# Kernel optimization log

Hardware: AMD Instinct MI355X
Metric: run time of the kernel (lower is better)

The kernel has to match this reference:

```python
import jax, jax.numpy as jnp
import numpy as np

D = 1024      # n_embd
NH = 16       # attention heads
E = 8         # n_experts
K = 2         # k_best
FF = 4 * D    # expert MLP hidden
EPS = 1e-6    # rms_norm_epsilon
TEMP = 1.0    # target_temperature


def setup_inputs() -> dict:
    key = jax.random.key(0)
    ks = jax.random.split(key, 12)
    B, S = 2, 1024
    s = 0.02
    return {
        "x": jax.random.normal(ks[0], (B, S, D), jnp.float32),
        "attn_norm_w": jnp.ones((D,), jnp.float32),
        "wq": jax.random.normal(ks[1], (D, D), jnp.float32) * s,
        "wk": jax.random.normal(ks[2], (D, D), jnp.float32) * s,
        "wv": jax.random.normal(ks[3], (D, D), jnp.float32) * s,
        "wo": jax.random.normal(ks[4], (D, D), jnp.float32) * s,
        "mlp_norm_w": jnp.ones((D,), jnp.float32),
        "router_w": jax.random.normal(ks[5], (D, E), jnp.float32) * s,
        "w1": jax.random.normal(ks[6], (E, D, FF), jnp.float32) * s,
        "b1": jnp.zeros((E, FF), jnp.float32),
        "w2": jax.random.normal(ks[7], (E, FF, D), jnp.float32) * s,
        "b2": jnp.zeros((E, D), jnp.float32),
    }


def _rmsnorm(x, w):
    var = jnp.mean(jnp.square(x), axis=-1, keepdims=True)
    return x * jax.lax.rsqrt(var + EPS) * w


def _attention(x, wq, wk, wv, wo):
    B, S, _ = x.shape
    dh = D // NH
    q = (x @ wq).reshape(B, S, NH, dh)
    k = (x @ wk).reshape(B, S, NH, dh)
    v = (x @ wv).reshape(B, S, NH, dh)
    scores = jnp.einsum("bqhd,bkhd->bhqk", q, k) / jnp.sqrt(jnp.float32(dh))
    causal = jnp.tril(jnp.ones((S, S), bool))  # [S,S]
    scores = jnp.where(causal[None, None], scores, jnp.finfo(scores.dtype).min)
    attn = jax.nn.softmax(scores, axis=-1)
    out = jnp.einsum("bhqk,bkhd->bqhd", attn, v).reshape(B, S, D)
    return out @ wo


def reference(x, attn_norm_w, wq, wk, wv, wo, mlp_norm_w, router_w, w1, b1, w2, b2):
    B, S, _ = x.shape
    # attention sub-block
    x = x + _attention(_rmsnorm(x, attn_norm_w), wq, wk, wv, wo)
    residual = x
    h = _rmsnorm(x, mlp_norm_w)  # [B,S,D]

    # router: temperature softmax + top-k
    logits = h @ router_w / TEMP                      # [B,S,E]
    probs = jax.nn.softmax(logits, axis=-1)
    top_k_scores, top_k_indices = jax.lax.top_k(probs, K)  # [B,S,K]
    onehot = jax.nn.one_hot(top_k_indices, E, dtype=h.dtype)  # [B,S,K,E]
    gates = jnp.einsum("bsk,bske->bse", top_k_scores, onehot)  # [B,S,E]

    # load-balancing loss (Switch-style) + expert counts
    counts = jnp.sum(onehot, axis=(0, 1, 2))          # [E]
    frac = counts / (B * S * K)
    mean_prob = jnp.mean(probs, axis=(0, 1))          # [E]
    balancing_loss = E * jnp.sum(frac * mean_prob)

    # experts: dense dispatch; tokens with zero gate contribute nothing,
    # so this matches the sort/gather/scatter top-k combine exactly.
    pre = jnp.einsum("bsd,edf->ebsf", h, w1) + b1[:, None, None]  # [E,B,S,FF]
    act = jax.nn.gelu(pre)
    y = jnp.einsum("ebsf,efd->ebsd", act, w2) + b2[:, None, None]  # [E,B,S,D]
    moe = jnp.einsum("ebsd,bse->bsd", y, gates)

    out = residual + moe
    return out, balancing_loss, counts
```

## Files before the change

kernel.cpp:

```cpp
#include <hip/hip_runtime.h>

typedef __bf16 bf16;
typedef __bf16 bf16x8 __attribute__((ext_vector_type(8)));
typedef float f32x4 __attribute__((ext_vector_type(4)));

#define D_   1024
#define S_   1024
#define B_   2
#define NTOK 2048
#define FF_  4096
#define NE   8
#define CAP  5120
#define OUTN 2097152

__device__ __forceinline__ float gelu_f(float x) {
    float u = 0.7978845608028654f * (x + 0.044715f * x * x * x);
    float a = fabsf(u);
    float e = __expf(-2.0f * a);
    float t = (1.0f - e) / (1.0f + e);
    t = copysignf(t, u);
    return 0.5f * x * (1.0f + t);
}

__device__ __forceinline__ void gload16(const void* g, void* l) {
    __builtin_amdgcn_global_load_lds((const __attribute__((address_space(1))) unsigned int*)g,
                                     (__attribute__((address_space(3))) unsigned int*)l,
                                     16, 0, 0);
}

#define VMCNT(n) asm volatile("s_waitcnt vmcnt(" n ")" ::: "memory")
#define BARRIER() do { asm volatile("" ::: "memory"); \
                       __builtin_amdgcn_s_barrier();  \
                       asm volatile("" ::: "memory"); } while (0)

__global__ __launch_bounds__(256) void rmsnorm_k(const float* __restrict__ x,
                                                 const float* __restrict__ w,
                                                 float* __restrict__ yf,
                                                 bf16* __restrict__ yhi,
                                                 bf16* __restrict__ ylo) {
    int row = blockIdx.x;
    int t = threadIdx.x;
    const float* xr = x + (size_t)row * D_;
    float4 v = *(const float4*)(xr + t * 4);
    float ss = v.x * v.x + v.y * v.y + v.z * v.z + v.w * v.w;
    for (int off = 32; off; off >>= 1) ss += __shfl_down(ss, off);
    __shared__ float wsum[4];
    if ((t & 63) == 0) wsum[t >> 6] = ss;
    __syncthreads();
    float tot = wsum[0] + wsum[1] + wsum[2] + wsum[3];
    float rr = rsqrtf(tot * (1.0f / D_) + 1e-6f);
    float4 wv = *(const float4*)(w + t * 4);
    float y[4];
    y[0] = v.x * rr * wv.x; y[1] = v.y * rr * wv.y;
    y[2] = v.z * rr * wv.z; y[3] = v.w * rr * wv.w;
    if (yf) *(float4*)(yf + (size_t)row * D_ + t * 4) = *(float4*)y;
    if (yhi) {
#pragma unroll
        for (int i = 0; i < 4; i++) {
            bf16 hi = (bf16)y[i];
            yhi[(size_t)row * D_ + t * 4 + i] = hi;
            if (ylo) ylo[(size_t)row * D_ + t * 4 + i] = (bf16)(y[i] - (float)hi);
        }
    }
}

__global__ __launch_bounds__(256) void trans_split_k(
    const float* __restrict__ w0, const float* __restrict__ w1p,
    const float* __restrict__ w2p, const float* __restrict__ w3,
    bf16* o0h, bf16* o0l, bf16* o1h, bf16* o1l,
    bf16* o2h, bf16* o2l, bf16* o3h, bf16* o3l) {
    int z = blockIdx.z;
    const float* src = (z == 0) ? w0 : (z == 1) ? w1p : (z == 2) ? w2p : w3;
    bf16* dh = (z == 0) ? o0h : (z == 1) ? o1h : (z == 2) ? o2h : o3h;
    bf16* dl = (z == 0) ? o0l : (z == 1) ? o1l : (z == 2) ? o2l : o3l;
    __shared__ float tl[32][33];
    int c0 = blockIdx.x * 32, r0 = blockIdx.y * 32;
    int tx = threadIdx.x & 31, ty = threadIdx.x >> 5;
#pragma unroll
    for (int i = 0; i < 4; i++) {
        int r = ty + i * 8;
        tl[r][tx] = src[(size_t)(r0 + r) * 1024 + c0 + tx];
    }
    __syncthreads();
#pragma unroll
    for (int i = 0; i < 4; i++) {
        int c = ty + i * 8;
        float v = tl[tx][c];
        bf16 hi = (bf16)v;
        dh[(size_t)(c0 + c) * 1024 + r0 + tx] = hi;
        dl[(size_t)(c0 + c) * 1024 + r0 + tx] = (bf16)(v - (float)hi);
    }
}

__global__ __launch_bounds__(256) void transpose_cast_k(const float* __restrict__ in,
                                                        bf16* __restrict__ out,
                                                        int R, int C) {
    __shared__ float tl[32][33];
    size_t base = (size_t)blockIdx.z * R * C;
    const float* src = in + base;
    bf16* dst = out + base;
    int c0 = blockIdx.x * 32, r0 = blockIdx.y * 32;
    int tx = threadIdx.x & 31, tyy = threadIdx.x >> 5;
#pragma unroll
    for (int i = 0; i < 4; i++) {
        int r = tyy + i * 8;
        tl[r][tx] = src[(size_t)(r0 + r) * C + c0 + tx];
    }
    __syncthreads();
#pragma unroll
    for (int i = 0; i < 4; i++) {
        int c = tyy + i * 8;
        dst[(size_t)(c0 + c) * R + r0 + tx] = (bf16)tl[tx][c];
    }
}

#define SPLIT_STAGE(bi, k0)                             \
    gload16(gah0 + (k0), Lah[bi] + wv * 512);           \
    gload16(gah1 + (k0), Lah[bi] + 2048 + wv * 512);    \
    gload16(gal0 + (k0), Lal[bi] + wv * 512);           \
    gload16(gal1 + (k0), Lal[bi] + 2048 + wv * 512);    \
    gload16(gbh0 + (k0), Lbh[bi] + wv * 512);           \
    gload16(gbh1 + (k0), Lbh[bi] + 2048 + wv * 512);    \
    gload16(gbl0 + (k0), Lbl[bi] + wv * 512);           \
    gload16(gbl1 + (k0), Lbl[bi] + 2048 + wv * 512);

#define SPLIT_COMPUTE(bi) {                                                            \
    bf16x8 fah[4], fal[4], fbh[4], fbl[4];                                             \
    _Pragma("unroll") for (int i = 0; i < 4; i++) {                                    \
        fah[i] = *(const bf16x8*)(Lah[bi] + ra_off[i]);                                \
        fal[i] = *(const bf16x8*)(Lal[bi] + ra_off[i]);                                \
        fbh[i] = *(const bf16x8*)(Lbh[bi] + rb_off[i]);                                \
        fbl[i] = *(const bf16x8*)(Lbl[bi] + rb_off[i]);                                \
    }                                                                                  \
    _Pragma("unroll") for (int mt = 0; mt < 4; mt++)                                   \
    _Pragma("unroll") for (int nt = 0; nt < 4; nt++) {                                 \
        acc[mt][nt] = __builtin_amdgcn_mfma_f32_16x16x32_bf16(fah[mt], fbh[nt], acc[mt][nt], 0, 0, 0); \
        acc[mt][nt] = __builtin_amdgcn_mfma_f32_16x16x32_bf16(fah[mt], fbl[nt], acc[mt][nt], 0, 0, 0); \
        acc[mt][nt] = __builtin_amdgcn_mfma_f32_16x16x32_bf16(fal[mt], fbh[nt], acc[mt][nt], 0, 0, 0); \
    } }

#define GEMM128_SPLIT_BODY(EPILOGUE)                                                   \
    __shared__ __align__(16) bf16 Lah[2][4096];                                        \
    __shared__ __align__(16) bf16 Lal[2][4096];                                        \
    __shared__ __align__(16) bf16 Lbh[2][4096];                                        \
    __shared__ __align__(16) bf16 Lbl[2][4096];                                        \
    int t = threadIdx.x;                                                               \
    int wv = t >> 6, ln = t & 63;                                                      \
    int wm = wv >> 1, wn = wv & 1, l15 = ln & 15, qd = ln >> 4;                        \
    int sr0 = t >> 2, sr1 = 64 + sr0, cl = t & 3;                                      \
    int cs0 = (cl ^ ((sr0 >> 1) & 3)) * 8;                                             \
    int cs1 = (cl ^ ((sr1 >> 1) & 3)) * 8;                                             \
    const bf16* gah0 = Ah + (size_t)(m0 + sr0) * 1024 + cs0;                           \
    const bf16* gah1 = Ah + (size_t)(m0 + sr1) * 1024 + cs1;                           \
    const bf16* gal0 = Al + (size_t)(m0 + sr0) * 1024 + cs0;                           \
    const bf16* gal1 = Al + (size_t)(m0 + sr1) * 1024 + cs1;                           \
    const bf16* gbh0 = Bh + (size_t)(n0 + sr0) * 1024 + cs0;                           \
    const bf16* gbh1 = Bh + (size_t)(n0 + sr1) * 1024 + cs1;                           \
    const bf16* gbl0 = Bl + (size_t)(n0 + sr0) * 1024 + cs0;                           \
    const bf16* gbl1 = Bl + (size_t)(n0 + sr1) * 1024 + cs1;                           \
    int ra_off[4], rb_off[4];                                                          \
    _Pragma("unroll") for (int i = 0; i < 4; i++) {                                    \
        int r1 = wm * 64 + i * 16 + l15;                                               \
        ra_off[i] = r1 * 32 + (qd ^ ((r1 >> 1) & 3)) * 8;                              \
        int r2 = wn * 64 + i * 16 + l15;                                               \
        rb_off[i] = r2 * 32 + (qd ^ ((r2 >> 1) & 3)) * 8;                              \
    }                                                                                  \
    f32x4 acc[4][4];                                                                   \
    _Pragma("unroll") for (int mt = 0; mt < 4; mt++)                                   \
    _Pragma("unroll") for (int nt = 0; nt < 4; nt++) acc[mt][nt] = (f32x4){0.f,0.f,0.f,0.f}; \
    SPLIT_STAGE(0, 0);                                                                 \
    __syncthreads();                                                                   \
    for (int k0 = 0; k0 < 1024; k0 += 64) {                                            \
        SPLIT_STAGE(1, k0 + 32);                                                       \
        SPLIT_COMPUTE(0);                                                              \
        __syncthreads();                                                               \
        if (k0 + 64 < 1024) { SPLIT_STAGE(0, k0 + 64); }                               \
        SPLIT_COMPUTE(1);                                                              \
        __syncthreads();                                                               \
    }                                                                                  \
    _Pragma("unroll") for (int mt = 0; mt < 4; mt++)                                   \
    _Pragma("unroll") for (int nt = 0; nt < 4; nt++)                                   \
        _Pragma("unroll") for (int r = 0; r < 4; r++) {                                \
            int gm = m0 + wm * 64 + mt * 16 + qd * 4 + r;                              \
            int gn = n0 + wn * 64 + nt * 16 + l15;                                     \
            float vv = acc[mt][nt][r];                                                 \
            EPILOGUE                                                                   \
        }

__global__ __launch_bounds__(256) void gemm_qkv_k(
    const bf16* __restrict__ Ah, const bf16* __restrict__ Al,
    const bf16* __restrict__ Bqh, const bf16* __restrict__ Bql,
    const bf16* __restrict__ Bkh, const bf16* __restrict__ Bkl,
    const bf16* __restrict__ Bvh, const bf16* __restrict__ Bvl,
    bf16* Cqh, bf16* Cql, bf16* Ckh, bf16* Ckl, bf16* Cvh, bf16* Cvl) {
    int gy = blockIdx.y, zw = gy >> 3;
    const bf16* Bh = (zw == 0) ? Bqh : (zw == 1) ? Bkh : Bvh;
    const bf16* Bl = (zw == 0) ? Bql : (zw == 1) ? Bkl : Bvl;
    bf16* Ch = (zw == 0) ? Cqh : (zw == 1) ? Ckh : Cvh;
    bf16* Cl = (zw == 0) ? Cql : (zw == 1) ? Ckl : Cvl;
    int m0 = blockIdx.x * 128, n0 = (gy & 7) * 128;
    GEMM128_SPLIT_BODY({
        bf16 hi = (bf16)vv;
        Ch[(size_t)gm * D_ + gn] = hi;
        Cl[(size_t)gm * D_ + gn] = (bf16)(vv - (float)hi);
    })
}

__global__ __launch_bounds__(256) void gemm_wo_k(
    const bf16* __restrict__ Ah, const bf16* __restrict__ Al,
    const bf16* __restrict__ Bh, const bf16* __restrict__ Bl,
    float* __restrict__ C, const float* __restrict__ X) {
    int m0 = blockIdx.x * 128, n0 = blockIdx.y * 128;
    GEMM128_SPLIT_BODY({
        C[(size_t)gm * D_ + gn] = X[(size_t)gm * D_ + gn] + vv;
    })
}

#define AP 72

__global__ __launch_bounds__(256) void attn_mfma_k(
    const bf16* __restrict__ qhp, const bf16* __restrict__ qlp,
    const bf16* __restrict__ khp, const bf16* __restrict__ klp,
    const bf16* __restrict__ vhp, const bf16* __restrict__ vlp,
    bf16* __restrict__ aoh, bf16* __restrict__ aol) {
    int qt = (int)gridDim.x - 1 - (int)blockIdx.x;
    int h = blockIdx.y, b = blockIdx.z;
    __shared__ bf16 Ksh[64 * AP], Ksl[64 * AP], VTh[64 * AP], VTl[64 * AP];
    __shared__ bf16 Ph[4][16 * AP], Pl[4][16 * AP];
    int t = threadIdx.x, wv = t >> 6, ln = t & 63, l15 = ln & 15, qd = ln >> 4;

    bf16x8 aqh[2], aql[2];
    {
        size_t qb = ((size_t)(b * S_ + qt * 64 + wv * 16 + l15)) * D_ + h * 64 + qd * 8;
        aqh[0] = *(const bf16x8*)(qhp + qb);
        aqh[1] = *(const bf16x8*)(qhp + qb + 32);
        aql[0] = *(const bf16x8*)(qlp + qb);
        aql[1] = *(const bf16x8*)(qlp + qb + 32);
    }
    f32x4 oacc[4];
    float mrow[4], lrow[4];
#pragma unroll
    for (int i = 0; i < 4; i++) {
        oacc[i] = (f32x4){0.f, 0.f, 0.f, 0.f};
        mrow[i] = -1e30f; lrow[i] = 0.0f;
    }

    for (int kt = 0; kt <= qt; kt++) {
        __syncthreads();
#pragma unroll
        for (int j = 0; j < 2; j++) {
            int idx = t + j * 256;
            int row = idx >> 3, ch = (idx & 7) * 8;
            size_t g = ((size_t)(b * S_ + kt * 64 + row)) * D_ + h * 64 + ch;
            *(bf16x8*)&Ksh[row * AP + ch] = *(const bf16x8*)(khp + g);
            *(bf16x8*)&Ksl[row * AP + ch] = *(const bf16x8*)(klp + g);
            bf16x8 vvh = *(const bf16x8*)(vhp + g);
            bf16x8 vvl = *(const bf16x8*)(vlp + g);
#pragma unroll
            for (int jj = 0; jj < 8; jj++) {
                VTh[(ch + jj) * AP + row] = vvh[jj];
                VTl[(ch + jj) * AP + row] = vvl[jj];
            }
        }
        __syncthreads();

        f32x4 sacc[4];
#pragma unroll
        for (int nt = 0; nt < 4; nt++) sacc[nt] = (f32x4){0.f, 0.f, 0.f, 0.f};
#pragma unroll
        for (int ks = 0; ks < 2; ks++) {
#pragma unroll
            for (int nt = 0; nt < 4; nt++) {
                bf16x8 bh = *(const bf16x8*)&Ksh[(nt * 16 + l15) * AP + ks * 32 + qd * 8];
                bf16x8 bl = *(const bf16x8*)&Ksl[(nt * 16 + l15) * AP + ks * 32 + qd * 8];
                sacc[nt] = __builtin_amdgcn_mfma_f32_16x16x32_bf16(aqh[ks], bh, sacc[nt], 0, 0, 0);
                sacc[nt] = __builtin_amdgcn_mfma_f32_16x16x32_bf16(aqh[ks], bl, sacc[nt], 0, 0, 0);
                sacc[nt] = __builtin_amdgcn_mfma_f32_16x16x32_bf16(aql[ks], bh, sacc[nt], 0, 0, 0);
            }
        }
        bool diag = (kt == qt);
#pragma unroll
        for (int r = 0; r < 4; r++) {
            float s0[4];
#pragma unroll
            for (int nt = 0; nt < 4; nt++) {
                s0[nt] = sacc[nt][r] * 0.125f;
                if (diag && (nt * 16 + l15) > (wv * 16 + qd * 4 + r)) s0[nt] = -1e30f;
            }
            float vmax = fmaxf(fmaxf(s0[0], s0[1]), fmaxf(s0[2], s0[3]));
            for (int off = 1; off < 16; off <<= 1) vmax = fmaxf(vmax, __shfl_xor(vmax, off));
            float mnew = fmaxf(mrow[r], vmax);
            float alpha = __expf(mrow[r] - mnew);
            float p[4], rs = 0.0f;
#pragma unroll
            for (int nt = 0; nt < 4; nt++) { p[nt] = __expf(s0[nt] - mnew); rs += p[nt]; }
            for (int off = 1; off < 16; off <<= 1) rs += __shfl_xor(rs, off);
            lrow[r] = lrow[r] * alpha + rs;
            mrow[r] = mnew;
#pragma unroll
            for (int nt = 0; nt < 4; nt++) oacc[nt][r] *= alpha;
            int prow = qd * 4 + r;
#pragma unroll
            for (int nt = 0; nt < 4; nt++) {
                bf16 hi = (bf16)p[nt];
                Ph[wv][prow * AP + nt * 16 + l15] = hi;
                Pl[wv][prow * AP + nt * 16 + l15] = (bf16)(p[nt] - (float)hi);
            }
        }
#pragma unroll
        for (int ks2 = 0; ks2 < 2; ks2++) {
            bf16x8 aph = *(const bf16x8*)&Ph[wv][l15 * AP + ks2 * 32 + qd * 8];
            bf16x8 apl = *(const bf16x8*)&Pl[wv][l15 * AP + ks2 * 32 + qd * 8];
#pragma unroll
            for (int nt = 0; nt < 4; nt++) {
                bf16x8 bvh = *(const bf16x8*)&VTh[(nt * 16 + l15) * AP + ks2 * 32 + qd * 8];
                bf16x8 bvl = *(const bf16x8*)&VTl[(nt * 16 + l15) * AP + ks2 * 32 + qd * 8];
                oacc[nt] = __builtin_amdgcn_mfma_f32_16x16x32_bf16(aph, bvh, oacc[nt], 0, 0, 0);
                oacc[nt] = __builtin_amdgcn_mfma_f32_16x16x32_bf16(aph, bvl, oacc[nt], 0, 0, 0);
                oacc[nt] = __builtin_amdgcn_mfma_f32_16x16x32_bf16(apl, bvh, oacc[nt], 0, 0, 0);
            }
        }
    }

#pragma unroll
    for (int r = 0; r < 4; r++) {
        float inv = 1.0f / lrow[r];
        size_t rowa = ((size_t)(b * S_ + qt * 64 + wv * 16 + qd * 4 + r)) * D_ + h * 64;
#pragma unroll
        for (int nt = 0; nt < 4; nt++) {
            float o = oacc[nt][r] * inv;
            bf16 hi = (bf16)o;
            aoh[rowa + nt * 16 + l15] = hi;
            aol[rowa + nt * 16 + l15] = (bf16)(o - (float)hi);
        }
    }
}

__global__ __launch_bounds__(256) void router_k(const float* __restrict__ h,
                                                const float* __restrict__ rw,
                                                int* __restrict__ tidx,
                                                float* __restrict__ tgate,
                                                int* __restrict__ ecnt,
                                                float* __restrict__ psum) {
    int wv = threadIdx.x >> 6, ln = threadIdx.x & 63;
    int tok = blockIdx.x * 4 + wv;
    const float* hr = h + (size_t)tok * D_;
    float acc[NE];
#pragma unroll
    for (int e = 0; e < NE; e++) acc[e] = 0.0f;
    int base = ln * 16;
#pragma unroll
    for (int c = 0; c < 4; c++) {
        float4 hv = *(const float4*)(hr + base + c * 4);
        const float* rp = rw + (size_t)(base + c * 4) * NE;
        float hx[4] = {hv.x, hv.y, hv.z, hv.w};
#pragma unroll
        for (int jj = 0; jj < 4; jj++)
#pragma unroll
            for (int e = 0; e < NE; e++)
                acc[e] = fmaf(hx[jj], rp[jj * NE + e], acc[e]);
    }
#pragma unroll
    for (int e = 0; e < NE; e++)
        for (int off = 32; off; off >>= 1) acc[e] += __shfl_down(acc[e], off);

    __shared__ float pb[4][NE];
    if (ln == 0) {
        float mx = acc[0];
#pragma unroll
        for (int e = 1; e < NE; e++) mx = fmaxf(mx, acc[e]);
        float p[NE], ssum = 0.0f;
#pragma unroll
        for (int e = 0; e < NE; e++) { p[e] = expf(acc[e] - mx); ssum += p[e]; }
        float inv = 1.0f / ssum;
#pragma unroll
        for (int e = 0; e < NE; e++) p[e] *= inv;
        int i0 = 0; float b0 = p[0];
#pragma unroll
        for (int e = 1; e < NE; e++) if (p[e] > b0) { b0 = p[e]; i0 = e; }
        int i1 = -1; float b1v = -1.0f;
#pragma unroll
        for (int e = 0; e < NE; e++) if (e != i0 && p[e] > b1v) { b1v = p[e]; i1 = e; }
        tidx[tok * 2] = i0; tidx[tok * 2 + 1] = i1;
        tgate[tok * 2] = b0; tgate[tok * 2 + 1] = b1v;
        atomicAdd(&ecnt[i0], 1);
        atomicAdd(&ecnt[i1], 1);
#pragma unroll
        for (int e = 0; e < NE; e++) pb[wv][e] = p[e];
    }
    __syncthreads();
    if (threadIdx.x < NE) {
        float s2 = pb[0][threadIdx.x] + pb[1][threadIdx.x] + pb[2][threadIdx.x] + pb[3][threadIdx.x];
        atomicAdd(&psum[threadIdx.x], s2);
    }
}

__global__ void passb_k(const int* __restrict__ ecnt, const float* __restrict__ psum,
                        int* __restrict__ eoffp, int* __restrict__ ecnt2,
                        float* __restrict__ out_tail) {
    if (threadIdx.x == 0) {
        int off = 0; float loss = 0.0f;
        for (int e = 0; e < NE; e++) {
            eoffp[e] = off;
            int c = ecnt[e];
            off += (c + 127) & ~127;
            loss += (c * (1.0f / 4096.0f)) * (psum[e] * (1.0f / 2048.0f));
            out_tail[1 + e] = (float)c;
            ecnt2[e] = 0;
        }
        eoffp[NE] = off;
        out_tail[0] = 8.0f * loss;
    }
}

__global__ __launch_bounds__(256) void scatter_k(const int* __restrict__ tidx,
                                                 const int* __restrict__ eoffp,
                                                 int* __restrict__ ecnt2,
                                                 int* __restrict__ stok,
                                                 int* __restrict__ sidx) {
    int tok = blockIdx.x * 256 + threadIdx.x;
    for (int k = 0; k < 2; k++) {
        int e = tidx[tok * 2 + k];
        int pos = eoffp[e] + atomicAdd(&ecnt2[e], 1);
        stok[pos] = tok;
        sidx[tok * 2 + k] = pos;
    }
}

#define MOE_STAGE(bufA, bufB, k0)                       \
    gload16(ga0 + (k0), (bufA) + wv * 512);             \
    gload16(ga1 + (k0), (bufA) + 2048 + wv * 512);      \
    gload16(gb0 + (k0), (bufB) + wv * 512);             \
    gload16(gb1 + (k0), (bufB) + 2048 + wv * 512);

#define MOE_TILE(bufA, bufB) {                                                         \
    bf16x8 af[4], bfr[4];                                                              \
    _Pragma("unroll") for (int i = 0; i < 4; i++) {                                    \
        af[i]  = *(const bf16x8*)((bufA) + ra_off[i]);                                 \
        bfr[i] = *(const bf16x8*)((bufB) + rb_off[i]);                                 \
    }                                                                                  \
    _Pragma("unroll") for (int mt = 0; mt < 4; mt++)                                   \
    _Pragma("unroll") for (int nt = 0; nt < 4; nt++)                                   \
        acc[mt][nt] = __builtin_amdgcn_mfma_f32_16x16x32_bf16(af[mt], bfr[nt], acc[mt][nt], 0, 0, 0); }

#define MOE_STEP(rdA, rdB, VM)      \
    VMCNT(VM);                      \
    BARRIER();                      \
    MOE_TILE(rdA, rdB);             \
    BARRIER();

__global__ __launch_bounds__(256) void moe_gemm1_k(const bf16* __restrict__ hB,
                                                   const bf16* __restrict__ w1t,
                                                   const float* __restrict__ b1,
                                                   const int* __restrict__ eoffp,
                                                   const int* __restrict__ stok,
                                                   bf16* __restrict__ act) {
    int m0 = blockIdx.x * 128, n0 = blockIdx.y * 128;
    if (m0 >= eoffp[NE]) return;
    int e = 0;
#pragma unroll
    for (int i = 1; i < NE; i++) if (m0 >= eoffp[i]) e = i;

    __shared__ __align__(16) bf16 As[2][4096];
    __shared__ __align__(16) bf16 Bs[2][4096];
    int t = threadIdx.x;
    int wv = t >> 6, ln = t & 63;
    int wm = wv >> 1, wn = wv & 1, l15 = ln & 15, qd = ln >> 4;

    int sr0 = t >> 2, sr1 = 64 + sr0, cl = t & 3;
    int cs0 = (cl ^ ((sr0 >> 1) & 3)) * 8;
    int cs1 = (cl ^ ((sr1 >> 1) & 3)) * 8;
    const bf16* ga0 = hB + (size_t)stok[m0 + sr0] * D_ + cs0;
    const bf16* ga1 = hB + (size_t)stok[m0 + sr1] * D_ + cs1;
    const bf16* Bb = w1t + ((size_t)e * FF_ + n0) * D_;
    const bf16* gb0 = Bb + (size_t)sr0 * D_ + cs0;
    const bf16* gb1 = Bb + (size_t)sr1 * D_ + cs1;

    int ra_off[4], rb_off[4];
#pragma unroll
    for (int i = 0; i < 4; i++) {
        int r1 = wm * 64 + i * 16 + l15;
        ra_off[i] = r1 * 32 + (qd ^ ((r1 >> 1) & 3)) * 8;
        int r2 = wn * 64 + i * 16 + l15;
        rb_off[i] = r2 * 32 + (qd ^ ((r2 >> 1) & 3)) * 8;
    }

    f32x4 acc[4][4];
#pragma unroll
    for (int mt = 0; mt < 4; mt++)
#pragma unroll
        for (int nt = 0; nt < 4; nt++) acc[mt][nt] = (f32x4){0.f, 0.f, 0.f, 0.f};

    MOE_STAGE(As[0], Bs[0], 0);
    for (int k0 = 0; k0 < 960; k0 += 64) {
        MOE_STAGE(As[1], Bs[1], k0 + 32);
        MOE_STEP(As[0], Bs[0], "4");
        MOE_STAGE(As[0], Bs[0], k0 + 64);
        MOE_STEP(As[1], Bs[1], "4");
    }
    MOE_STAGE(As[1], Bs[1], 992);
    MOE_STEP(As[0], Bs[0], "4");
    MOE_STEP(As[1], Bs[1], "0");

    const float* b1e = b1 + (size_t)e * FF_;
#pragma unroll
    for (int mt = 0; mt < 4; mt++)
#pragma unroll
        for (int nt = 0; nt < 4; nt++) {
            int gn = n0 + wn * 64 + nt * 16 + l15;
            float bias = b1e[gn];
#pragma unroll
            for (int r = 0; r < 4; r++) {
                int gm = m0 + wm * 64 + mt * 16 + qd * 4 + r;
                act[(size_t)gm * FF_ + gn] = (bf16)gelu_f(acc[mt][nt][r] + bias);
            }
        }
}

__global__ __launch_bounds__(256) void moe_gemm2_k(const bf16* __restrict__ act,
                                                   const bf16* __restrict__ w2t,
                                                   const float* __restrict__ b2,
                                                   const int* __restrict__ eoffp,
                                                   float* __restrict__ y) {
    int m0 = blockIdx.x * 128, n0 = blockIdx.y * 128;
    if (m0 >= eoffp[NE]) return;
    int e = 0;
#pragma unroll
    for (int i = 1; i < NE; i++) if (m0 >= eoffp[i]) e = i;

    __shared__ __align__(16) bf16 As[4][4096];
    __shared__ __align__(16) bf16 Bs[4][4096];
    int t = threadIdx.x;
    int wv = t >> 6, ln = t & 63;
    int wm = wv >> 1, wn = wv & 1, l15 = ln & 15, qd = ln >> 4;

    int sr0 = t >> 2, sr1 = 64 + sr0, cl = t & 3;
    int cs0 = (cl ^ ((sr0 >> 1) & 3)) * 8;
    int cs1 = (cl ^ ((sr1 >> 1) & 3)) * 8;
    const bf16* ga0 = act + (size_t)(m0 + sr0) * FF_ + cs0;
    const bf16* ga1 = act + (size_t)(m0 + sr1) * FF_ + cs1;
    const bf16* Bb = w2t + ((size_t)e * D_ + n0) * FF_;
    const bf16* gb0 = Bb + (size_t)sr0 * FF_ + cs0;
    const bf16* gb1 = Bb + (size_t)sr1 * FF_ + cs1;

    int ra_off[4], rb_off[4];
#pragma unroll
    for (int i = 0; i < 4; i++) {
        int r1 = wm * 64 + i * 16 + l15;
        ra_off[i] = r1 * 32 + (qd ^ ((r1 >> 1) & 3)) * 8;
        int r2 = wn * 64 + i * 16 + l15;
        rb_off[i] = r2 * 32 + (qd ^ ((r2 >> 1) & 3)) * 8;
    }

    f32x4 acc[4][4];
#pragma unroll
    for (int mt = 0; mt < 4; mt++)
#pragma unroll
        for (int nt = 0; nt < 4; nt++) acc[mt][nt] = (f32x4){0.f, 0.f, 0.f, 0.f};

    MOE_STAGE(As[0], Bs[0], 0);
    MOE_STAGE(As[1], Bs[1], 32);
    for (int k0 = 0; k0 < 3968; k0 += 128) {
        MOE_STAGE(As[2], Bs[2], k0 + 64);  MOE_STEP(As[0], Bs[0], "8");
        MOE_STAGE(As[3], Bs[3], k0 + 96);  MOE_STEP(As[1], Bs[1], "8");
        MOE_STAGE(As[0], Bs[0], k0 + 128); MOE_STEP(As[2], Bs[2], "8");
        MOE_STAGE(As[1], Bs[1], k0 + 160); MOE_STEP(As[3], Bs[3], "8");
    }
    MOE_STAGE(As[2], Bs[2], 4032); MOE_STEP(As[0], Bs[0], "8");
    MOE_STAGE(As[3], Bs[3], 4064); MOE_STEP(As[1], Bs[1], "8");
    MOE_STEP(As[2], Bs[2], "4");
    MOE_STEP(As[3], Bs[3], "0");

    const float* b2e = b2 + (size_t)e * D_;
#pragma unroll
    for (int mt = 0; mt < 4; mt++)
#pragma unroll
        for (int nt = 0; nt < 4; nt++) {
            int gn = n0 + wn * 64 + nt * 16 + l15;
            float bias = b2e[gn];
#pragma unroll
            for (int r = 0; r < 4; r++) {
                int gm = m0 + wm * 64 + mt * 16 + qd * 4 + r;
                y[(size_t)gm * D_ + gn] = acc[mt][nt][r] + bias;
            }
        }
}

__global__ __launch_bounds__(256) void combine_k(const float* __restrict__ y,
                                                 const int* __restrict__ sidx,
                                                 const float* __restrict__ tgate,
                                                 float* __restrict__ out) {
    int tok = blockIdx.x;
    int d = threadIdx.x * 4;
    int s0 = sidx[tok * 2], s1 = sidx[tok * 2 + 1];
    float g0 = tgate[tok * 2], g1 = tgate[tok * 2 + 1];
    float4 a = *(const float4*)(y + (size_t)s0 * D_ + d);
    float4 b = *(const float4*)(y + (size_t)s1 * D_ + d);
    float4 o = *(const float4*)(out + (size_t)tok * D_ + d);
    o.x += g0 * a.x + g1 * b.x;
    o.y += g0 * a.y + g1 * b.y;
    o.z += g0 * a.z + g1 * b.z;
    o.w += g0 * a.w + g1 * b.w;
    *(float4*)(out + (size_t)tok * D_ + d) = o;
}

extern "C" void kernel_launch(void* const* d_in, const int* in_sizes, int n_in,
                              void* d_out, int out_size, void* d_ws, size_t ws_size,
                              hipStream_t stream) {
    const float* x   = (const float*)d_in[0];
    const float* anw = (const float*)d_in[1];
    const float* wq  = (const float*)d_in[2];
    const float* wk  = (const float*)d_in[3];
    const float* wv  = (const float*)d_in[4];
    const float* wo  = (const float*)d_in[5];
    const float* mnw = (const float*)d_in[6];
    const float* rw  = (const float*)d_in[7];
    const float* w1  = (const float*)d_in[8];
    const float* b1  = (const float*)d_in[9];
    const float* w2  = (const float*)d_in[10];
    const float* b2  = (const float*)d_in[11];
    float* out = (float*)d_out;

    char* p = (char*)d_ws;
    auto take = [&](size_t n) { char* r = p; p += (n + 255) & ~(size_t)255; return r; };
    bf16* h1h = (bf16*)take((size_t)OUTN * 2);
    bf16* h1l = (bf16*)take((size_t)OUTN * 2);
    bf16* qh  = (bf16*)take((size_t)OUTN * 2);
    bf16* ql  = (bf16*)take((size_t)OUTN * 2);
    bf16* kh  = (bf16*)take((size_t)OUTN * 2);
    bf16* kl  = (bf16*)take((size_t)OUTN * 2);
    bf16* vh  = (bf16*)take((size_t)OUTN * 2);
    bf16* vl  = (bf16*)take((size_t)OUTN * 2);
    bf16* wqth = (bf16*)take((size_t)D_ * D_ * 2);
    bf16* wqtl = (bf16*)take((size_t)D_ * D_ * 2);
    bf16* wkth = (bf16*)take((size_t)D_ * D_ * 2);
    bf16* wktl = (bf16*)take((size_t)D_ * D_ * 2);
    bf16* wvth = (bf16*)take((size_t)D_ * D_ * 2);
    bf16* wvtl = (bf16*)take((size_t)D_ * D_ * 2);
    bf16* woth = (bf16*)take((size_t)D_ * D_ * 2);
    bf16* wotl = (bf16*)take((size_t)D_ * D_ * 2);
    bf16* w1t = (bf16*)take((size_t)NE * FF_ * D_ * 2);
    bf16* w2t = (bf16*)take((size_t)NE * FF_ * D_ * 2);
    bf16* act = (bf16*)take((size_t)CAP * FF_ * 2);
    int*   tidx  = (int*)take(NTOK * 2 * 4);
    float* tgate = (float*)take(NTOK * 2 * 4);
    int*   sidx  = (int*)take(NTOK * 2 * 4);
    int*   ecnt  = (int*)take(64);
    int*   ecnt2 = (int*)take(64);
    float* psum  = (float*)take(64);
    int*   eoffp = (int*)take(64);
    int*   stok  = (int*)take(CAP * 4);

    bf16*  aoh = h1h;
    bf16*  aol = h1l;
    float* h_f = (float*)qh;
    bf16*  h_b = kh;
    float* y   = (float*)vh;

    hipMemsetAsync(ecnt, 0, NE * 4, stream);
    hipMemsetAsync(psum, 0, NE * 4, stream);
    hipMemsetAsync(stok, 0, CAP * 4, stream);

    trans_split_k<<<dim3(32, 32, 4), 256, 0, stream>>>(wq, wk, wv, wo,
        wqth, wqtl, wkth, wktl, wvth, wvtl, woth, wotl);
    transpose_cast_k<<<dim3(FF_ / 32, D_ / 32, NE), 256, 0, stream>>>(w1, w1t, D_, FF_);
    transpose_cast_k<<<dim3(D_ / 32, FF_ / 32, NE), 256, 0, stream>>>(w2, w2t, FF_, D_);

    rmsnorm_k<<<NTOK, 256, 0, stream>>>(x, anw, nullptr, h1h, h1l);
    gemm_qkv_k<<<dim3(16, 24), 256, 0, stream>>>(h1h, h1l,
        wqth, wqtl, wkth, wktl, wvth, wvtl, qh, ql, kh, kl, vh, vl);
    attn_mfma_k<<<dim3(16, 16, 2), 256, 0, stream>>>(qh, ql, kh, kl, vh, vl, aoh, aol);
    gemm_wo_k<<<dim3(16, 8), 256, 0, stream>>>(aoh, aol, woth, wotl, out, x);

    rmsnorm_k<<<NTOK, 256, 0, stream>>>(out, mnw, h_f, h_b, nullptr);
    router_k<<<NTOK / 4, 256, 0, stream>>>(h_f, rw, tidx, tgate, ecnt, psum);
    passb_k<<<1, 64, 0, stream>>>(ecnt, psum, eoffp, ecnt2, out + OUTN);
    scatter_k<<<NTOK / 256, 256, 0, stream>>>(tidx, eoffp, ecnt2, stok, sidx);
    moe_gemm1_k<<<dim3(CAP / 128, FF_ / 128), 256, 0, stream>>>(h_b, w1t, b1, eoffp, stok, act);
    moe_gemm2_k<<<dim3(CAP / 128, D_ / 128), 256, 0, stream>>>(act, w2t, b2, eoffp, y);
    combine_k<<<NTOK, 256, 0, stream>>>(y, sidx, tgate, out);
}
```

Baseline: 790.6 us.

## Split-K the second MoE GEMM and vectorize weight transpose-cast kernels

The second expert GEMM is split along K into two halves via a third grid dimension, and the partial results are accumulated into a zero-initialized output with float atomics. The bias is added only by the first half. This doubles the block count for a grid that previously had few tiles (40x8), at the cost of a memset of the output buffer and atomic read-modify-write traffic. Separately, the w1/w2 transpose-cast kernel now uses 64x64 tiles with float4 loads and 4-wide bf16 stores to cut memory transactions.

After: 795.7 us. Within noise of the previous version (+0.6%).

```diff
diff --git a/kernel.cpp b/kernel.cpp
--- a/kernel.cpp
+++ b/kernel.cpp
@@ -1,6 +1,7 @@
 #include <hip/hip_runtime.h>
 
 typedef __bf16 bf16;
+typedef __bf16 bf16x4 __attribute__((ext_vector_type(4)));
 typedef __bf16 bf16x8 __attribute__((ext_vector_type(8)));
 typedef float f32x4 __attribute__((ext_vector_type(4)));
 
@@ -92,25 +93,33 @@
     }
 }
 
-__global__ __launch_bounds__(256) void transpose_cast_k(const float* __restrict__ in,
-                                                        bf16* __restrict__ out,
-                                                        int R, int C) {
-    __shared__ float tl[32][33];
+__global__ __launch_bounds__(256) void transpose_cast4_k(const float* __restrict__ in,
+                                                         bf16* __restrict__ out,
+                                                         int R, int C) {
+    __shared__ float tl[64][65];
     size_t base = (size_t)blockIdx.z * R * C;
     const float* src = in + base;
     bf16* dst = out + base;
-    int c0 = blockIdx.x * 32, r0 = blockIdx.y * 32;
-    int tx = threadIdx.x & 31, tyy = threadIdx.x >> 5;
+    int c0 = blockIdx.x * 64, r0 = blockIdx.y * 64;
+    int t = threadIdx.x;
+    int lr = t >> 4;
+    int lc = (t & 15) * 4;
 #pragma unroll
     for (int i = 0; i < 4; i++) {
-        int r = tyy + i * 8;
-        tl[r][tx] = src[(size_t)(r0 + r) * C + c0 + tx];
+        int r = lr + i * 16;
+        float4 v = *(const float4*)(src + (size_t)(r0 + r) * C + c0 + lc);
+        tl[r][lc] = v.x; tl[r][lc + 1] = v.y; tl[r][lc + 2] = v.z; tl[r][lc + 3] = v.w;
     }
     __syncthreads();
+    int wc = t >> 4;
+    int wr = (t & 15) * 4;
 #pragma unroll
     for (int i = 0; i < 4; i++) {
-        int c = tyy + i * 8;
-        dst[(size_t)(c0 + c) * R + r0 + tx] = (bf16)tl[tx][c];
+        int c = wc + i * 16;
+        bf16x4 o;
+        o[0] = (bf16)tl[wr][c];     o[1] = (bf16)tl[wr + 1][c];
+        o[2] = (bf16)tl[wr + 2][c]; o[3] = (bf16)tl[wr + 3][c];
+        *(bf16x4*)(dst + (size_t)(c0 + c) * R + r0 + wr) = o;
     }
 }
 
@@ -527,6 +536,8 @@
     int e = 0;
 #pragma unroll
     for (int i = 1; i < NE; i++) if (m0 >= eoffp[i]) e = i;
+    int zk = blockIdx.z;
+    int kbase = zk * 2048;
 
     __shared__ __align__(16) bf16 As[4][4096];
     __shared__ __align__(16) bf16 Bs[4][4096];
@@ -537,11 +548,11 @@
     int sr0 = t >> 2, sr1 = 64 + sr0, cl = t & 3;
     int cs0 = (cl ^ ((sr0 >> 1) & 3)) * 8;
     int cs1 = (cl ^ ((sr1 >> 1) & 3)) * 8;
-    const bf16* ga0 = act + (size_t)(m0 + sr0) * FF_ + cs0;
-    const bf16* ga1 = act + (size_t)(m0 + sr1) * FF_ + cs1;
+    const bf16* ga0 = act + (size_t)(m0 + sr0) * FF_ + kbase + cs0;
+    const bf16* ga1 = act + (size_t)(m0 + sr1) * FF_ + kbase + cs1;
     const bf16* Bb = w2t + ((size_t)e * D_ + n0) * FF_;
-    const bf16* gb0 = Bb + (size_t)sr0 * FF_ + cs0;
-    const bf16* gb1 = Bb + (size_t)sr1 * FF_ + cs1;
+    const bf16* gb0 = Bb + (size_t)sr0 * FF_ + kbase + cs0;
+    const bf16* gb1 = Bb + (size_t)sr1 * FF_ + kbase + cs1;
 
     int ra_off[4], rb_off[4];
 #pragma unroll
@@ -560,14 +571,14 @@
 
     MOE_STAGE(As[0], Bs[0], 0);
     MOE_STAGE(As[1], Bs[1], 32);
-    for (int k0 = 0; k0 < 3968; k0 += 128) {
+    for (int k0 = 0; k0 < 1920; k0 += 128) {
         MOE_STAGE(As[2], Bs[2], k0 + 64);  MOE_STEP(As[0], Bs[0], "8");
         MOE_STAGE(As[3], Bs[3], k0 + 96);  MOE_STEP(As[1], Bs[1], "8");
         MOE_STAGE(As[0], Bs[0], k0 + 128); MOE_STEP(As[2], Bs[2], "8");
         MOE_STAGE(As[1], Bs[1], k0 + 160); MOE_STEP(As[3], Bs[3], "8");
     }
-    MOE_STAGE(As[2], Bs[2], 4032); MOE_STEP(As[0], Bs[0], "8");
-    MOE_STAGE(As[3], Bs[3], 4064); MOE_STEP(As[1], Bs[1], "8");
+    MOE_STAGE(As[2], Bs[2], 1984); MOE_STEP(As[0], Bs[0], "8");
+    MOE_STAGE(As[3], Bs[3], 2016); MOE_STEP(As[1], Bs[1], "8");
     MOE_STEP(As[2], Bs[2], "4");
     MOE_STEP(As[3], Bs[3], "0");
 
@@ -577,11 +588,11 @@
 #pragma unroll
         for (int nt = 0; nt < 4; nt++) {
             int gn = n0 + wn * 64 + nt * 16 + l15;
-            float bias = b2e[gn];
+            float bias = (zk == 0) ? b2e[gn] : 0.0f;
 #pragma unroll
             for (int r = 0; r < 4; r++) {
                 int gm = m0 + wm * 64 + mt * 16 + qd * 4 + r;
-                y[(size_t)gm * D_ + gn] = acc[mt][nt][r] + bias;
+                atomicAdd(&y[(size_t)gm * D_ + gn], acc[mt][nt][r] + bias);
             }
         }
 }
@@ -663,8 +674,8 @@
 
     trans_split_k<<<dim3(32, 32, 4), 256, 0, stream>>>(wq, wk, wv, wo,
         wqth, wqtl, wkth, wktl, wvth, wvtl, woth, wotl);
-    transpose_cast_k<<<dim3(FF_ / 32, D_ / 32, NE), 256, 0, stream>>>(w1, w1t, D_, FF_);
-    transpose_cast_k<<<dim3(D_ / 32, FF_ / 32, NE), 256, 0, stream>>>(w2, w2t, FF_, D_);
+    transpose_cast4_k<<<dim3(FF_ / 64, D_ / 64, NE), 256, 0, stream>>>(w1, w1t, D_, FF_);
+    transpose_cast4_k<<<dim3(D_ / 64, FF_ / 64, NE), 256, 0, stream>>>(w2, w2t, FF_, D_);
 
     rmsnorm_k<<<NTOK, 256, 0, stream>>>(x, anw, nullptr, h1h, h1l);
     gemm_qkv_k<<<dim3(16, 24), 256, 0, stream>>>(h1h, h1l,
@@ -672,11 +683,12 @@
     attn_mfma_k<<<dim3(16, 16, 2), 256, 0, stream>>>(qh, ql, kh, kl, vh, vl, aoh, aol);
     gemm_wo_k<<<dim3(16, 8), 256, 0, stream>>>(aoh, aol, woth, wotl, out, x);
 
+    hipMemsetAsync(y, 0, (size_t)CAP * D_ * 4, stream);
     rmsnorm_k<<<NTOK, 256, 0, stream>>>(out, mnw, h_f, h_b, nullptr);
     router_k<<<NTOK / 4, 256, 0, stream>>>(h_f, rw, tidx, tgate, ecnt, psum);
     passb_k<<<1, 64, 0, stream>>>(ecnt, psum, eoffp, ecnt2, out + OUTN);
     scatter_k<<<NTOK / 256, 256, 0, stream>>>(tidx, eoffp, ecnt2, stok, sidx);
     moe_gemm1_k<<<dim3(CAP / 128, FF_ / 128), 256, 0, stream>>>(h_b, w1t, b1, eoffp, stok, act);
-    moe_gemm2_k<<<dim3(CAP / 128, D_ / 128), 256, 0, stream>>>(act, w2t, b2, eoffp, y);
+    moe_gemm2_k<<<dim3(CAP / 128, D_ / 128, 2), 256, 0, stream>>>(act, w2t, b2, eoffp, y);
     combine_k<<<NTOK, 256, 0, stream>>>(y, sidx, tgate, out);
 }
```
